# Kernel optimization log

Measured on AMD Instinct MI355X. Metric: run time of the kernel, lower is better.

Reference implementation:

```python
import jax, jax.numpy as jnp
import numpy as np

NB = 32          # num_basis
RMAX = 2.5       # max_radius
M0, M1 = 16, 8   # multiplicities of 0e and 1o irreps

# normalize2mom constant for silu (makes E[act(x)^2]=1 under N(0,1)), as in e3nn FullyConnectedNet
_p, _w = np.polynomial.hermite_e.hermegauss(128)
_s = _p / (1.0 + np.exp(-_p))
SILU_C = float(1.0 / np.sqrt((_w * _s * _s).sum() / np.sqrt(2.0 * np.pi)))

INV3 = 1.0 / np.sqrt(3.0)   # w3j(1,1,0)=w3j(0,1,1)=w3j(1,0,1) coefficient
INV6 = 1.0 / np.sqrt(6.0)   # w3j(1,1,1) = eps_ijk/sqrt(6)
PW0 = float(np.sqrt(1.0 / (M0 + M1)))        # path weight -> 0e (component/element norm)
PW1 = float(np.sqrt(3.0 / (M0 + M1 + M1)))   # path weight -> 1o
PW_SIM = float(np.sqrt(1.0 / (M0 * M0 + M1 * M1)))  # similarity TP path weight


def basis_net(rb, W1, W2):
    # e3nn FullyConnectedNet([NB,16,numel], silu): x@W/sqrt(fan_in), normalized act, linear out
    h = SILU_C * jax.nn.silu(rb @ (W1 / np.sqrt(NB)))
    return h @ (W2 / np.sqrt(16.0))


def fc_tp(x0, x1, sh0, sh1, w):
    # FullyConnectedTensorProduct (16x0e+8x1o) x (0e+1o) -> (16x0e+8x1o), per-edge weights
    # x0 [E,16], x1 [E,8,3], sh0 [E], sh1 [E,3], w [E,640]
    E = w.shape[0]
    w0 = w[:, 0:256].reshape(E, M0, M0)    # 0e x 0e -> 0e
    w1 = w[:, 256:384].reshape(E, M0, M1)  # 0e x 1o -> 1o
    w2 = w[:, 384:448].reshape(E, M1, M1)  # 1o x 0e -> 1o
    w3 = w[:, 448:576].reshape(E, M1, M0)  # 1o x 1o -> 0e
    w4 = w[:, 576:640].reshape(E, M1, M1)  # 1o x 1o -> 1o
    dot = jnp.einsum('eui,ei->eu', x1, sh1)
    out0 = PW0 * (jnp.einsum('euw,eu->ew', w0, x0 * sh0[:, None])
                  + INV3 * jnp.einsum('euw,eu->ew', w3, dot))
    crx = jnp.cross(x1, sh1[:, None, :])
    out1 = PW1 * (INV3 * jnp.einsum('euw,eu,ei->ewi', w1, x0, sh1)
                  + INV3 * sh0[:, None, None] * jnp.einsum('euw,eui->ewi', w2, x1)
                  + INV6 * jnp.einsum('euw,eui->ewi', w4, crx))
    return out0, out1


def forward(x, pos, edge_src, edge_dst, w_key1, w_key2, w_val1, w_val2, w_q0, w_q1, w_sim0, w_sim1):
    N = x.shape[0]
    x0 = x[:, :M0]                       # [N,16] scalars
    x1 = x[:, M0:].reshape(N, M1, 3)     # [N,8,3] vectors
    vec = pos[edge_src] - pos[edge_dst]  # [E,3]
    r = jnp.sqrt((vec * vec).sum(-1) + 1e-12)
    # bessel soft_one_hot_linspace with cutoff, scaled by sqrt(num_basis)
    n = jnp.arange(1, NB + 1, dtype=x.dtype) * jnp.pi
    rb = jnp.sqrt(2.0 / RMAX) * jnp.sin(n * (r[:, None] / RMAX)) / r[:, None]
    rb = jnp.where(r[:, None] < RMAX, rb, 0.0) * np.sqrt(1.0 * NB)
    # spherical harmonics lmax=1, normalize=True, normalization='component'
    unit = vec / r[:, None]
    sh0 = jnp.ones_like(r)
    sh1 = np.sqrt(3.0) * unit
    # query projection (o3.Linear, per-irrep dense / sqrt(fan_in))
    q0 = x0 @ (w_q0 / np.sqrt(M0))
    q1 = jnp.einsum('nui,uv->nvi', x1, w_q1) / np.sqrt(M1)
    x0s, x1s = x0[edge_src], x1[edge_src]
    k0, k1 = fc_tp(x0s, x1s, sh0, sh1, basis_net(rb, w_key1, w_key2))
    v0, v1 = fc_tp(x0s, x1s, sh0, sh1, basis_net(rb, w_val1, w_val2))
    # similarity TP (q,k)->0e
    s = PW_SIM * (jnp.einsum('eu,uv,ev->e', q0[edge_dst], w_sim0, k0)
                  + INV3 * jnp.einsum('eui,uv,evi->e', q1[edge_dst], w_sim1, k1))
    # scatter softmax over incoming edges per dst node
    smax = jax.ops.segment_max(s, edge_dst, num_segments=N)
    ex = jnp.exp(s - smax[edge_dst])
    attn = ex / jax.ops.segment_sum(ex, edge_dst, num_segments=N)[edge_dst]
    coef = jnp.sqrt(jax.nn.relu(attn))
    vals = jnp.concatenate([v0, v1.reshape(-1, 3 * M1)], axis=-1)  # [E,40]
    return jax.ops.segment_sum(coef[:, None] * vals, edge_dst, num_segments=N)


def setup_inputs() -> dict:
    key = jax.random.key(0)
    ks = jax.random.split(key, 12)
    N, E = 16384, 262144
    return dict(
        x=jax.random.normal(ks[0], (N, 40), jnp.float32),
        pos=jax.random.uniform(ks[1], (N, 3), jnp.float32) * 2.0,  # box so r spans cutoff
        edge_src=jax.random.randint(ks[2], (E,), 0, N, jnp.int32),
        edge_dst=jax.random.randint(ks[3], (E,), 0, N, jnp.int32),
        w_key1=jax.random.normal(ks[4], (32, 16), jnp.float32),
        w_key2=jax.random.normal(ks[5], (16, 640), jnp.float32),
        w_val1=jax.random.normal(ks[6], (32, 16), jnp.float32),
        w_val2=jax.random.normal(ks[7], (16, 640), jnp.float32),
        w_q0=jax.random.normal(ks[8], (16, 16), jnp.float32),
        w_q1=jax.random.normal(ks[9], (8, 8), jnp.float32),
        w_sim0=jax.random.normal(ks[10], (16, 16), jnp.float32),
        w_sim1=jax.random.normal(ks[11], (8, 8), jnp.float32),
    )


def reference(x, pos, edge_src, edge_dst, w_key1, w_key2, w_val1, w_val2, w_q0, w_q1, w_sim0, w_sim1):
    return forward(x, pos, edge_src, edge_dst, w_key1, w_key2, w_val1, w_val2, w_q0, w_q1, w_sim0, w_sim1)
```

## Files before the change

kernel.cpp:

```cpp
#include <hip/hip_runtime.h>
#include <math.h>

#define TPB 256
#define TPBF 192
#define SRCS_PER_GRP 8
#define SRC_STRIDE_U16 1928

#define RMAX_F 2.5f
#define PI_F 3.14159265358979323846f
#define SQRT3_F 1.7320508075688772f
#define INV3_F 0.5773502691896258f
#define INV6_F 0.4082482904638631f
#define PW0_F 0.2041241452319315f
#define PW1_F 0.3061862178478972f
#define PWSIM_F 0.05590169943749474f
#define SILU_C_F 1.676866f
#define RB_F 0.8944271909999159f
#define INV_SQRT8_F 0.35355339059327373f

typedef unsigned short u16t;
typedef _Float16 f16x2 __attribute__((ext_vector_type(2)));

#if defined(__has_builtin)
#if __has_builtin(__builtin_amdgcn_fdot2)
#define HAVE_FDOT2 1
#else
#define HAVE_FDOT2 0
#endif
#else
#define HAVE_FDOT2 0
#endif


__device__ __forceinline__ f16x2 as_f16x2(int v) {
  union { int i; f16x2 h; } u; u.i = v; return u.h;
}
__device__ __forceinline__ unsigned f16x2_bits(f16x2 h) {
  union { f16x2 h; unsigned u; } c; c.h = h; return c.u;
}
__device__ __forceinline__ float f16b2f(u16t b) {
  union { u16t u; _Float16 h; } c; c.u = b; return (float)c.h;
}

__device__ __forceinline__ float dot2f16(f16x2 a, f16x2 b, float c) {
#if HAVE_FDOT2
  return __builtin_amdgcn_fdot2(a, b, c, false);
#else
  return fmaf((float)a.x, (float)b.x, fmaf((float)a.y, (float)b.y, c));
#endif
}

__device__ __forceinline__ float dotjh(const u16t* __restrict__ t,
                                       const f16x2* __restrict__ hp) {
  const int4* q = reinterpret_cast<const int4*>(t);
  int4 a = q[0], b = q[1];
  float s0 = 0.f, s1 = 0.f;
  s0 = dot2f16(as_f16x2(a.x), hp[0], s0);
  s1 = dot2f16(as_f16x2(a.y), hp[1], s1);
  s0 = dot2f16(as_f16x2(a.z), hp[2], s0);
  s1 = dot2f16(as_f16x2(a.w), hp[3], s1);
  s0 = dot2f16(as_f16x2(b.x), hp[4], s0);
  s1 = dot2f16(as_f16x2(b.y), hp[5], s1);
  s0 = dot2f16(as_f16x2(b.z), hp[6], s0);
  s1 = dot2f16(as_f16x2(b.w), hp[7], s1);
  return s0 + s1;
}

__device__ __forceinline__ void pack_h16(const float* __restrict__ h,
                                         f16x2* __restrict__ hp) {
#pragma unroll
  for (int i = 0; i < 8; ++i) {
    f16x2 v;
    v.x = (_Float16)h[2 * i + 0];
    v.y = (_Float16)h[2 * i + 1];
    hp[i] = v;
  }
}

__device__ __forceinline__ float dot16u(const float* __restrict__ w, const float* __restrict__ h) {
  float a0 = 0.f, a1 = 0.f, a2 = 0.f, a3 = 0.f;
#pragma unroll
  for (int j = 0; j < 16; j += 4) {
    a0 = fmaf(h[j + 0], w[j + 0], a0);
    a1 = fmaf(h[j + 1], w[j + 1], a1);
    a2 = fmaf(h[j + 2], w[j + 2], a2);
    a3 = fmaf(h[j + 3], w[j + 3], a3);
  }
  return (a0 + a1) + (a2 + a3);
}

__device__ __forceinline__ void compute_h2s(const float* __restrict__ pos,
                                            const float* __restrict__ W1k,
                                            const float* __restrict__ W1v,
                                            int src, int dst,
                                            float& shx, float& shy, float& shz,
                                            float hk[16], float hv[16]) {
  float vx = pos[3 * src + 0] - pos[3 * dst + 0];
  float vy = pos[3 * src + 1] - pos[3 * dst + 1];
  float vz = pos[3 * src + 2] - pos[3 * dst + 2];
  float r2 = fmaf(vx, vx, fmaf(vy, vy, vz * vz)) + 1e-12f;
  float r = sqrtf(r2);
  float inv_r = 1.0f / r;
  shx = SQRT3_F * vx * inv_r;
  shy = SQRT3_F * vy * inv_r;
  shz = SQRT3_F * vz * inv_r;
  float f = (r < RMAX_F) ? (RB_F * inv_r) : 0.0f;
  float t0 = (PI_F / RMAX_F) * r;
  float s1, c1;
  __sincosf(t0, &s1, &c1);
  float c2 = 2.0f * c1;
  float sm = 0.0f, sc = s1;
  float ak[16], av[16];
#pragma unroll
  for (int j = 0; j < 16; ++j) { ak[j] = 0.0f; av[j] = 0.0f; }
#pragma unroll 2
  for (int n = 0; n < 32; ++n) {
    float rb = f * sc;
    const float* wk = W1k + n * 16;
    const float* wv = W1v + n * 16;
#pragma unroll
    for (int j = 0; j < 16; ++j) ak[j] = fmaf(rb, wk[j], ak[j]);
#pragma unroll
    for (int j = 0; j < 16; ++j) av[j] = fmaf(rb, wv[j], av[j]);
    float nx = fmaf(c2, sc, -sm);
    sm = sc; sc = nx;
  }
#pragma unroll
  for (int j = 0; j < 16; ++j) {
    float v = ak[j];
    hk[j] = SILU_C_F * v * (1.0f / (1.0f + __expf(-v)));
    float w = av[j];
    hv[j] = SILU_C_F * w * (1.0f / (1.0f + __expf(-w)));
  }
}

__device__ __forceinline__ void gen_entry_h(const u16t* __restrict__ W2H,
                                            const unsigned* __restrict__ xh,
                                            int mm, unsigned outw[8]) {
  f16x2 acc[8];
#pragma unroll
  for (int i = 0; i < 8; ++i) { acc[i].x = (_Float16)0.f; acc[i].y = (_Float16)0.f; }
  if (mm < 16) {
    int w = mm;
#pragma unroll 1
    for (int u = 0; u < 16; ++u) {
      f16x2 xv = as_f16x2((int)xh[u]);
      const f16x2* wp = reinterpret_cast<const f16x2*>(W2H + (u * 16 + w) * 16);
#pragma unroll
      for (int i = 0; i < 8; ++i) acc[i] += xv * wp[i];
    }
  } else if (mm < 24) {
    int w = mm - 16;
#pragma unroll 1
    for (int u = 0; u < 16; ++u) {
      f16x2 xv = as_f16x2((int)xh[u]);
      const f16x2* wp = reinterpret_cast<const f16x2*>(W2H + (256 + u * 8 + w) * 16);
#pragma unroll
      for (int i = 0; i < 8; ++i) acc[i] += xv * wp[i];
    }
  } else if (mm < 48) {
    int tt = mm - 24, w = tt / 3, i3 = tt - w * 3;
#pragma unroll 1
    for (int u = 0; u < 8; ++u) {
      f16x2 xv = as_f16x2((int)xh[16 + u * 3 + i3]);
      const f16x2* wp = reinterpret_cast<const f16x2*>(W2H + (384 + u * 8 + w) * 16);
#pragma unroll
      for (int i = 0; i < 8; ++i) acc[i] += xv * wp[i];
    }
  } else if (mm < 96) {
    int tt = mm - 48, w = tt / 3, i3 = tt - w * 3;
#pragma unroll 1
    for (int u = 0; u < 8; ++u) {
      f16x2 xv = as_f16x2((int)xh[16 + u * 3 + i3]);
      const f16x2* wp = reinterpret_cast<const f16x2*>(W2H + (448 + u * 16 + w) * 16);
#pragma unroll
      for (int i = 0; i < 8; ++i) acc[i] += xv * wp[i];
    }
  } else {
    int tt = mm - 96, w = tt / 3, i3 = tt - w * 3;
#pragma unroll 1
    for (int u = 0; u < 8; ++u) {
      f16x2 xv = as_f16x2((int)xh[16 + u * 3 + i3]);
      const f16x2* wp = reinterpret_cast<const f16x2*>(W2H + (576 + u * 8 + w) * 16);
#pragma unroll
      for (int i = 0; i < 8; ++i) acc[i] += xv * wp[i];
    }
  }
#pragma unroll
  for (int i = 0; i < 8; ++i) outw[i] = f16x2_bits(acc[i]);
}

__device__ __forceinline__ void gen_tables(const u16t* __restrict__ W2H,
                                           const unsigned* __restrict__ xh,
                                           u16t* __restrict__ tl,
                                           int nsrc, int tid) {
  for (int idx = tid; idx < nsrc * 120; idx += TPBF) {
    int m, s;
    if (nsrc == SRCS_PER_GRP) {
      m = idx >> 3;
      s = idx & 7;
    } else {
      m = idx / nsrc;
      s = idx - m * nsrc;
    }
    unsigned r[8];
    gen_entry_h(W2H, xh + s * 40, m, r);
    int4* dp = reinterpret_cast<int4*>(&tl[s * SRC_STRIDE_U16 + m * 16]);
    dp[0] = make_int4((int)r[0], (int)r[1], (int)r[2], (int)r[3]);
    dp[1] = make_int4((int)r[4], (int)r[5], (int)r[6], (int)r[7]);
  }
}


__global__ void k_prep(const float* __restrict__ wk2, const float* __restrict__ wv2,
                       const float* __restrict__ wq0, const float* __restrict__ wq1,
                       const float* __restrict__ ws0, const float* __restrict__ ws1,
                       float* __restrict__ W2Tk, float* __restrict__ W2Tv,
                       u16t* __restrict__ W2Hk, u16t* __restrict__ W2Hv,
                       float* __restrict__ C0, float* __restrict__ C1) {
  int i = blockIdx.x * blockDim.x + threadIdx.x;
  if (i < 10240) {
    int o = i >> 4, j = i & 15;
    float v = wk2[j * 640 + o] * 0.25f;
    W2Tk[i] = v;
    union { _Float16 h; u16t u; } c; c.h = (_Float16)v;
    W2Hk[i] = c.u;
  } else if (i < 20480) {
    int k = i - 10240;
    int o = k >> 4, j = k & 15;
    float v = wv2[j * 640 + o] * 0.25f;
    W2Tv[k] = v;
    union { _Float16 h; u16t u; } c; c.h = (_Float16)v;
    W2Hv[k] = c.u;
  } else if (i < 20736) {
    int k = i - 20480;
    int t = k >> 4, v = k & 15;
    float a = 0.f;
#pragma unroll
    for (int u = 0; u < 16; ++u) a = fmaf(wq0[t * 16 + u] * 0.25f, ws0[u * 16 + v], a);
    C0[k] = a;
  } else if (i < 20800) {
    int k = i - 20736;
    int t = k >> 3, v = k & 7;
    float a = 0.f;
#pragma unroll
    for (int u = 0; u < 8; ++u) a = fmaf(wq1[t * 8 + u] * INV_SQRT8_F, ws1[u * 8 + v], a);
    C1[k] = a;
  }
}

__global__ void k_node(const float* __restrict__ x, const float* __restrict__ C0,
                       const float* __restrict__ C1, float* __restrict__ qs0g,
                       float* __restrict__ qs1g, int N) {
  int n = blockIdx.x * blockDim.x + threadIdx.x;
  if (n >= N) return;
  float xr[40];
  const float4* p = reinterpret_cast<const float4*>(x + (size_t)n * 40);
#pragma unroll
  for (int q = 0; q < 10; ++q) {
    float4 v = p[q];
    xr[q * 4 + 0] = v.x; xr[q * 4 + 1] = v.y; xr[q * 4 + 2] = v.z; xr[q * 4 + 3] = v.w;
  }
  float o0[16];
#pragma unroll
  for (int v = 0; v < 16; ++v) o0[v] = 0.f;
#pragma unroll
  for (int t = 0; t < 16; ++t) {
    float xt = xr[t];
    const float* c = C0 + t * 16;
#pragma unroll
    for (int v = 0; v < 16; ++v) o0[v] = fmaf(xt, c[v], o0[v]);
  }
  float4* q0p = reinterpret_cast<float4*>(qs0g + (size_t)n * 16);
#pragma unroll
  for (int q = 0; q < 4; ++q)
    q0p[q] = make_float4(o0[q * 4], o0[q * 4 + 1], o0[q * 4 + 2], o0[q * 4 + 3]);

  float o1[24];
#pragma unroll
  for (int v = 0; v < 24; ++v) o1[v] = 0.f;
#pragma unroll
  for (int u = 0; u < 8; ++u) {
    const float* c = C1 + u * 8;
    float xa = xr[16 + u * 3 + 0], xb = xr[16 + u * 3 + 1], xc = xr[16 + u * 3 + 2];
#pragma unroll
    for (int v = 0; v < 8; ++v) {
      float cv = c[v];
      o1[v * 3 + 0] = fmaf(xa, cv, o1[v * 3 + 0]);
      o1[v * 3 + 1] = fmaf(xb, cv, o1[v * 3 + 1]);
      o1[v * 3 + 2] = fmaf(xc, cv, o1[v * 3 + 2]);
    }
  }
  float4* q1p = reinterpret_cast<float4*>(qs1g + (size_t)n * 24);
#pragma unroll
  for (int q = 0; q < 6; ++q)
    q1p[q] = make_float4(o1[q * 4], o1[q * 4 + 1], o1[q * 4 + 2], o1[q * 4 + 3]);
}


__global__ void k_hist2(const int* __restrict__ esrc, const int* __restrict__ edst,
                        int* __restrict__ cnt_s, int* __restrict__ cnt_d, int E) {
  int e = blockIdx.x * blockDim.x + threadIdx.x;
  if (e < E) {
    atomicAdd(&cnt_s[esrc[e]], 1);
    atomicAdd(&cnt_d[edst[e]], 1);
  }
}

__global__ void k_hist1(const int* __restrict__ key, int* __restrict__ cnt, int E) {
  int e = blockIdx.x * blockDim.x + threadIdx.x;
  if (e < E) atomicAdd(&cnt[key[e]], 1);
}

__global__ __launch_bounds__(1024) void k_scan2(const int* __restrict__ cnt_s,
                                                int* __restrict__ off_s,
                                                int* __restrict__ cur_s,
                                                const int* __restrict__ cnt_d,
                                                int* __restrict__ off_d,
                                                int* __restrict__ cur_d, int N) {
  const int* __restrict__ cnt = blockIdx.x ? cnt_d : cnt_s;
  int* __restrict__ off = blockIdx.x ? off_d : off_s;
  int* __restrict__ cur = blockIdx.x ? cur_d : cur_s;
  __shared__ int ls[1024];
  int tid = threadIdx.x;
  int per = (N + 1023) >> 10;
  int base = tid * per;
  int sum = 0;
  for (int j = 0; j < per; ++j) {
    int idx = base + j;
    if (idx < N) sum += cnt[idx];
  }
  ls[tid] = sum;
  __syncthreads();
  for (int d = 1; d < 1024; d <<= 1) {
    int v = (tid >= d) ? ls[tid - d] : 0;
    __syncthreads();
    ls[tid] += v;
    __syncthreads();
  }
  int run = ls[tid] - sum;
  for (int j = 0; j < per; ++j) {
    int idx = base + j;
    if (idx < N) {
      off[idx] = run;
      cur[idx] = run;
      run += cnt[idx];
    }
  }
  if (tid == 1023) off[N] = run;
}

__global__ void k_place2(const int* __restrict__ esrc, const int* __restrict__ edst,
                         int* __restrict__ cur_s, int* __restrict__ cur_d,
                         int* __restrict__ perm, int* __restrict__ idx, int E) {
  int e = blockIdx.x * blockDim.x + threadIdx.x;
  if (e < E) {
    int p = atomicAdd(&cur_s[esrc[e]], 1);
    perm[p] = e;
    int q = atomicAdd(&cur_d[edst[e]], 1);
    idx[q] = p;
  }
}

__global__ void k_place(const int* __restrict__ key, int* __restrict__ cursor,
                        int* __restrict__ perm, int E) {
  int e = blockIdx.x * blockDim.x + threadIdx.x;
  if (e < E) {
    int p = atomicAdd(&cursor[key[e]], 1);
    perm[p] = e;
  }
}


__global__ __launch_bounds__(TPBF) void k_fused(
    const float* __restrict__ x, const float* __restrict__ pos,
    const int* __restrict__ esrc, const int* __restrict__ edst,
    const int* __restrict__ perm, const int* __restrict__ off_s,
    const float* __restrict__ W1k, const u16t* __restrict__ W2Hk,
    const float* __restrict__ W1v, const u16t* __restrict__ W2Hv,
    const float* __restrict__ qs0g, const float* __restrict__ qs1g,
    float* __restrict__ s_out, u16t* __restrict__ stg, int N) {
  __shared__ __align__(16) u16t tl[SRCS_PER_GRP * SRC_STRIDE_U16];
  __shared__ unsigned xh[SRCS_PER_GRP * 40];
  int tid = threadIdx.x;
  int base = blockIdx.x * SRCS_PER_GRP;
  int nsrc = min(SRCS_PER_GRP, N - base);
  int glo = off_s[base], ghi = off_s[base + nsrc];

  for (int idx = tid; idx < nsrc * 40; idx += TPBF) {
    int s = idx / 40, u = idx - s * 40;
    float v = x[(size_t)(base + s) * 40 + u];
    f16x2 hh; hh.x = (_Float16)v; hh.y = hh.x;
    xh[s * 40 + u] = f16x2_bits(hh);
  }
  __syncthreads();

  gen_tables(W2Hk, xh, tl, nsrc, tid);
  __syncthreads();

  for (int p0 = glo; p0 < ghi; p0 += TPBF) {
    int p = p0 + tid;
    bool act = p < ghi;

    float shx = 0.f, shy = 0.f, shz = 0.f;
    int sloc = 0;
    f16x2 hvp[8];
#pragma unroll
    for (int j = 0; j < 8; ++j) { hvp[j].x = (_Float16)0.f; hvp[j].y = (_Float16)0.f; }

    if (act) {
      int e = perm[p];
      int src = esrc[e];
      int dst = edst[e];
      sloc = src - base;
      float hk[16], hv[16];
      compute_h2s(pos, W1k, W1v, src, dst, shx, shy, shz, hk, hv);
      f16x2 hkp[8];
      pack_h16(hk, hkp);
      pack_h16(hv, hvp);

      const u16t* tk = &tl[sloc * SRC_STRIDE_U16];
      const float4* q0p = reinterpret_cast<const float4*>(qs0g + (size_t)dst * 16);
      float S0 = 0.f;
#pragma unroll 2
      for (int w4 = 0; w4 < 4; ++w4) {
        float4 qq = q0p[w4];
        float q[4] = {qq.x, qq.y, qq.z, qq.w};
#pragma unroll
        for (int k = 0; k < 4; ++k) {
          float t0 = dotjh(tk + (w4 * 4 + k) * 16, hkp);
          float t3x = dotjh(tk + (48 + w4 * 12 + k * 3 + 0) * 16, hkp);
          float t3y = dotjh(tk + (48 + w4 * 12 + k * 3 + 1) * 16, hkp);
          float t3z = dotjh(tk + (48 + w4 * 12 + k * 3 + 2) * 16, hkp);
          S0 = fmaf(q[k], fmaf(INV3_F, t3x * shx + t3y * shy + t3z * shz, t0), S0);
        }
      }
      const float4* q1p = reinterpret_cast<const float4*>(qs1g + (size_t)dst * 24);
      float S1 = 0.f;
#pragma unroll 2
      for (int w4 = 0; w4 < 2; ++w4) {
        float4 qa = q1p[w4 * 3 + 0];
        float4 qb = q1p[w4 * 3 + 1];
        float4 qc = q1p[w4 * 3 + 2];
        float q[12] = {qa.x, qa.y, qa.z, qa.w, qb.x, qb.y, qb.z, qb.w,
                       qc.x, qc.y, qc.z, qc.w};
#pragma unroll
        for (int k = 0; k < 4; ++k) {
          float qx = q[k * 3 + 0], qy = q[k * 3 + 1], qz = q[k * 3 + 2];
          float t1 = dotjh(tk + (16 + w4 * 4 + k) * 16, hkp);
          float t2x = dotjh(tk + (24 + w4 * 12 + k * 3 + 0) * 16, hkp);
          float t2y = dotjh(tk + (24 + w4 * 12 + k * 3 + 1) * 16, hkp);
          float t2z = dotjh(tk + (24 + w4 * 12 + k * 3 + 2) * 16, hkp);
          float c0 = dotjh(tk + (96 + w4 * 12 + k * 3 + 0) * 16, hkp);
          float c1 = dotjh(tk + (96 + w4 * 12 + k * 3 + 1) * 16, hkp);
          float c2 = dotjh(tk + (96 + w4 * 12 + k * 3 + 2) * 16, hkp);
          float crx = c1 * shz - c2 * shy;
          float cry = c2 * shx - c0 * shz;
          float crz = c0 * shy - c1 * shx;
          float qdots = qx * shx + qy * shy + qz * shz;
          S1 += INV3_F * (t1 * qdots + t2x * qx + t2y * qy + t2z * qz) +
                INV6_F * (crx * qx + cry * qy + crz * qz);
        }
      }
      s_out[p] = PWSIM_F * (PW0_F * S0 + PW1_F * INV3_F * S1);
    }
    __syncthreads();

    gen_tables(W2Hv, xh, tl, nsrc, tid);
    __syncthreads();

    if (act) {
      const u16t* tv = &tl[sloc * SRC_STRIDE_U16];
      u16t* sp = stg + (size_t)p * 40;
#pragma unroll 2
      for (int w4 = 0; w4 < 4; ++w4) {
        float f[4];
#pragma unroll
        for (int k = 0; k < 4; ++k) {
          float t0 = dotjh(tv + (w4 * 4 + k) * 16, hvp);
          float t3x = dotjh(tv + (48 + w4 * 12 + k * 3 + 0) * 16, hvp);
          float t3y = dotjh(tv + (48 + w4 * 12 + k * 3 + 1) * 16, hvp);
          float t3z = dotjh(tv + (48 + w4 * 12 + k * 3 + 2) * 16, hvp);
          f[k] = PW0_F * fmaf(INV3_F, t3x * shx + t3y * shy + t3z * shz, t0);
        }
        f16x2 pa; pa.x = (_Float16)f[0]; pa.y = (_Float16)f[1];
        f16x2 pb; pb.x = (_Float16)f[2]; pb.y = (_Float16)f[3];
        int2 pk;
        pk.x = (int)f16x2_bits(pa);
        pk.y = (int)f16x2_bits(pb);
        *reinterpret_cast<int2*>(sp + w4 * 4) = pk;
      }
#pragma unroll 2
      for (int w4 = 0; w4 < 2; ++w4) {
        float f[12];
#pragma unroll
        for (int k = 0; k < 4; ++k) {
          float t1 = dotjh(tv + (16 + w4 * 4 + k) * 16, hvp);
          float t2x = dotjh(tv + (24 + w4 * 12 + k * 3 + 0) * 16, hvp);
          float t2y = dotjh(tv + (24 + w4 * 12 + k * 3 + 1) * 16, hvp);
          float t2z = dotjh(tv + (24 + w4 * 12 + k * 3 + 2) * 16, hvp);
          float c0 = dotjh(tv + (96 + w4 * 12 + k * 3 + 0) * 16, hvp);
          float c1 = dotjh(tv + (96 + w4 * 12 + k * 3 + 1) * 16, hvp);
          float c2 = dotjh(tv + (96 + w4 * 12 + k * 3 + 2) * 16, hvp);
          float crx = c1 * shz - c2 * shy;
          float cry = c2 * shx - c0 * shz;
          float crz = c0 * shy - c1 * shx;
          f[k * 3 + 0] = PW1_F * (INV3_F * fmaf(t1, shx, t2x) + INV6_F * crx);
          f[k * 3 + 1] = PW1_F * (INV3_F * fmaf(t1, shy, t2y) + INV6_F * cry);
          f[k * 3 + 2] = PW1_F * (INV3_F * fmaf(t1, shz, t2z) + INV6_F * crz);
        }
#pragma unroll
        for (int g = 0; g < 3; ++g) {
          f16x2 pa; pa.x = (_Float16)f[g * 4 + 0]; pa.y = (_Float16)f[g * 4 + 1];
          f16x2 pb; pb.x = (_Float16)f[g * 4 + 2]; pb.y = (_Float16)f[g * 4 + 3];
          int2 pk;
          pk.x = (int)f16x2_bits(pa);
          pk.y = (int)f16x2_bits(pb);
          *reinterpret_cast<int2*>(sp + 16 + w4 * 12 + g * 4) = pk;
        }
      }
    }

    if (p0 + TPBF < ghi) {
      __syncthreads();
      gen_tables(W2Hk, xh, tl, nsrc, tid);
      __syncthreads();
    }
  }
}


__global__ void k_smg(const float* __restrict__ s, const u16t* __restrict__ stg,
                      const int* __restrict__ off, const int* __restrict__ idx,
                      float* __restrict__ out, int N) {
  int gid = blockIdx.x * blockDim.x + threadIdx.x;
  int wid = gid >> 6;
  int lane = threadIdx.x & 63;
  if (wid >= N) return;
  int lo = off[wid], hi = off[wid + 1];
  float m = -1e30f;
  for (int q = lo + lane; q < hi; q += 64) m = fmaxf(m, s[idx[q]]);
#pragma unroll
  for (int d = 32; d; d >>= 1) m = fmaxf(m, __shfl_xor(m, d));
  float sum = 0.f;
  for (int q = lo + lane; q < hi; q += 64) sum += __expf(s[idx[q]] - m);
#pragma unroll
  for (int d = 32; d; d >>= 1) sum += __shfl_xor(sum, d);
  float inv = 1.0f / sum;
  float acc = 0.f;
  for (int q0 = lo; q0 < hi; q0 += 64) {
    int q = q0 + lane;
    int pv = 0;
    float cv = 0.f;
    if (q < hi) {
      pv = idx[q];
      cv = sqrtf(__expf(s[pv] - m) * inv);
    }
    int nj = min(64, hi - q0);
    for (int j = 0; j < nj; ++j) {
      float cj = __shfl(cv, j);
      int pj = __shfl(pv, j);
      if (lane < 40)
        acc = fmaf(cj, f16b2f(stg[(size_t)pj * 40 + lane]), acc);
    }
  }
  if (lane < 40) out[(size_t)wid * 40 + lane] = acc;
}


__global__ __launch_bounds__(TPB) void k_edge_fused(
    const float* __restrict__ x, const float* __restrict__ pos,
    const int* __restrict__ esrc, const int* __restrict__ edst,
    const int* __restrict__ perm,
    const float* __restrict__ W1k, const float* __restrict__ W2Tk,
    const float* __restrict__ W1v, const float* __restrict__ W2Tv,
    const float* __restrict__ qs0g, const float* __restrict__ qs1g,
    float* __restrict__ s_out, float* __restrict__ staging, int E) {
  __shared__ float xs[TPB * 41];
  int p = blockIdx.x * TPB + threadIdx.x;
  if (p >= E) return;
  int e = perm[p];
  int src = esrc[e], dst = edst[e];

  float* myx = &xs[threadIdx.x * 41];
  const float4* xrow = reinterpret_cast<const float4*>(x + (size_t)src * 40);
#pragma unroll
  for (int q = 0; q < 10; ++q) {
    float4 v = xrow[q];
    myx[q * 4 + 0] = v.x; myx[q * 4 + 1] = v.y; myx[q * 4 + 2] = v.z; myx[q * 4 + 3] = v.w;
  }

  float sh1[3], hk[16], hv[16];
  compute_h2s(pos, W1k, W1v, src, dst, sh1[0], sh1[1], sh1[2], hk, hv);

  {
    float qs0[16];
    {
      const float4* qp = reinterpret_cast<const float4*>(qs0g + (size_t)dst * 16);
#pragma unroll
      for (int q = 0; q < 4; ++q) {
        float4 v = qp[q];
        qs0[q * 4 + 0] = v.x; qs0[q * 4 + 1] = v.y; qs0[q * 4 + 2] = v.z; qs0[q * 4 + 3] = v.w;
      }
    }
    float qs1[24];
    {
      const float4* qp = reinterpret_cast<const float4*>(qs1g + (size_t)dst * 24);
#pragma unroll
      for (int q = 0; q < 6; ++q) {
        float4 v = qp[q];
        qs1[q * 4 + 0] = v.x; qs1[q * 4 + 1] = v.y; qs1[q * 4 + 2] = v.z; qs1[q * 4 + 3] = v.w;
      }
    }
    float qsh[8];
#pragma unroll
    for (int w = 0; w < 8; ++w)
      qsh[w] = qs1[w * 3] * sh1[0] + qs1[w * 3 + 1] * sh1[1] + qs1[w * 3 + 2] * sh1[2];

    float S0a = 0.f, S0b = 0.f, S1a = 0.f, S1b = 0.f, S1c = 0.f;
#pragma unroll 1
    for (int u = 0; u < 16; ++u) {
      const float* base = W2Tk + (u * 16) * 16;
      float accu = 0.f;
#pragma unroll
      for (int w = 0; w < 16; ++w) accu = fmaf(dot16u(base + w * 16, hk), qs0[w], accu);
      S0a = fmaf(accu, myx[u], S0a);
    }
#pragma unroll 1
    for (int u = 0; u < 16; ++u) {
      const float* base = W2Tk + (256 + u * 8) * 16;
      float accu = 0.f;
#pragma unroll
      for (int w = 0; w < 8; ++w) accu = fmaf(dot16u(base + w * 16, hk), qsh[w], accu);
      S1a = fmaf(accu, myx[u], S1a);
    }
#pragma unroll 1
    for (int u = 0; u < 8; ++u) {
      const float* base = W2Tk + (384 + u * 8) * 16;
      float x1a = myx[16 + u * 3 + 0], x1b = myx[16 + u * 3 + 1], x1c = myx[16 + u * 3 + 2];
      float accu = 0.f;
#pragma unroll
      for (int w = 0; w < 8; ++w) {
        float t = qs1[w * 3] * x1a + qs1[w * 3 + 1] * x1b + qs1[w * 3 + 2] * x1c;
        accu = fmaf(dot16u(base + w * 16, hk), t, accu);
      }
      S1b += accu;
    }
#pragma unroll 1
    for (int u = 0; u < 8; ++u) {
      const float* base = W2Tk + (448 + u * 16) * 16;
      float x1a = myx[16 + u * 3 + 0], x1b = myx[16 + u * 3 + 1], x1c = myx[16 + u * 3 + 2];
      float du = x1a * sh1[0] + x1b * sh1[1] + x1c * sh1[2];
      float accu = 0.f;
#pragma unroll
      for (int w = 0; w < 16; ++w) accu = fmaf(dot16u(base + w * 16, hk), qs0[w], accu);
      S0b = fmaf(accu, du, S0b);
    }
#pragma unroll 1
    for (int u = 0; u < 8; ++u) {
      const float* base = W2Tk + (576 + u * 8) * 16;
      float x1a = myx[16 + u * 3 + 0], x1b = myx[16 + u * 3 + 1], x1c = myx[16 + u * 3 + 2];
      float cx = x1b * sh1[2] - x1c * sh1[1];
      float cy = x1c * sh1[0] - x1a * sh1[2];
      float cz = x1a * sh1[1] - x1b * sh1[0];
      float accu = 0.f;
#pragma unroll
      for (int w = 0; w < 8; ++w) {
        float t = qs1[w * 3] * cx + qs1[w * 3 + 1] * cy + qs1[w * 3 + 2] * cz;
        accu = fmaf(dot16u(base + w * 16, hk), t, accu);
      }
      S1c += accu;
    }
    s_out[p] = PWSIM_F * (PW0_F * (S0a + INV3_F * S0b) +
                          (INV3_F * PW1_F) * (INV3_F * S1a + INV3_F * S1b + INV6_F * S1c));
  }

  float v0[16];
#pragma unroll
  for (int w = 0; w < 16; ++w) v0[w] = 0.f;
  float v1[24];
#pragma unroll
  for (int w = 0; w < 24; ++w) v1[w] = 0.f;

#pragma unroll 1
  for (int u = 0; u < 16; ++u) {
    const float* base = W2Tv + (u * 16) * 16;
    float xu = myx[u];
#pragma unroll
    for (int w = 0; w < 16; ++w) v0[w] = fmaf(dot16u(base + w * 16, hv), xu, v0[w]);
  }
  {
    float aw[8];
#pragma unroll
    for (int w = 0; w < 8; ++w) aw[w] = 0.f;
#pragma unroll 1
    for (int u = 0; u < 16; ++u) {
      const float* base = W2Tv + (256 + u * 8) * 16;
      float xu = myx[u];
#pragma unroll
      for (int w = 0; w < 8; ++w) aw[w] = fmaf(dot16u(base + w * 16, hv), xu, aw[w]);
    }
#pragma unroll
    for (int w = 0; w < 8; ++w) {
      float t = INV3_F * aw[w];
      v1[w * 3 + 0] = fmaf(t, sh1[0], v1[w * 3 + 0]);
      v1[w * 3 + 1] = fmaf(t, sh1[1], v1[w * 3 + 1]);
      v1[w * 3 + 2] = fmaf(t, sh1[2], v1[w * 3 + 2]);
    }
  }
#pragma unroll 1
  for (int u = 0; u < 8; ++u) {
    const float* base = W2Tv + (384 + u * 8) * 16;
    float a0 = INV3_F * myx[16 + u * 3 + 0];
    float a1 = INV3_F * myx[16 + u * 3 + 1];
    float a2 = INV3_F * myx[16 + u * 3 + 2];
#pragma unroll
    for (int w = 0; w < 8; ++w) {
      float wk = dot16u(base + w * 16, hv);
      v1[w * 3 + 0] = fmaf(wk, a0, v1[w * 3 + 0]);
      v1[w * 3 + 1] = fmaf(wk, a1, v1[w * 3 + 1]);
      v1[w * 3 + 2] = fmaf(wk, a2, v1[w * 3 + 2]);
    }
  }
#pragma unroll 1
  for (int u = 0; u < 8; ++u) {
    const float* base = W2Tv + (448 + u * 16) * 16;
    float x1a = myx[16 + u * 3 + 0], x1b = myx[16 + u * 3 + 1], x1c = myx[16 + u * 3 + 2];
    float du = INV3_F * (x1a * sh1[0] + x1b * sh1[1] + x1c * sh1[2]);
#pragma unroll
    for (int w = 0; w < 16; ++w) v0[w] = fmaf(dot16u(base + w * 16, hv), du, v0[w]);
  }
#pragma unroll 1
  for (int u = 0; u < 8; ++u) {
    const float* base = W2Tv + (576 + u * 8) * 16;
    float x1a = myx[16 + u * 3 + 0], x1b = myx[16 + u * 3 + 1], x1c = myx[16 + u * 3 + 2];
    float cx = INV6_F * (x1b * sh1[2] - x1c * sh1[1]);
    float cy = INV6_F * (x1c * sh1[0] - x1a * sh1[2]);
    float cz = INV6_F * (x1a * sh1[1] - x1b * sh1[0]);
#pragma unroll
    for (int w = 0; w < 8; ++w) {
      float wk = dot16u(base + w * 16, hv);
      v1[w * 3 + 0] = fmaf(wk, cx, v1[w * 3 + 0]);
      v1[w * 3 + 1] = fmaf(wk, cy, v1[w * 3 + 1]);
      v1[w * 3 + 2] = fmaf(wk, cz, v1[w * 3 + 2]);
    }
  }

  float outv[40];
#pragma unroll
  for (int w = 0; w < 16; ++w) outv[w] = PW0_F * v0[w];
#pragma unroll
  for (int w = 0; w < 24; ++w) outv[16 + w] = PW1_F * v1[w];
  float4* st = reinterpret_cast<float4*>(staging + (size_t)p * 40);
#pragma unroll
  for (int q = 0; q < 10; ++q)
    st[q] = make_float4(outv[q * 4], outv[q * 4 + 1], outv[q * 4 + 2], outv[q * 4 + 3]);
}

__global__ void k_softmax(const float* __restrict__ s, const int* __restrict__ off,
                          float* __restrict__ coef, int N) {
  int gid = blockIdx.x * blockDim.x + threadIdx.x;
  int wid = gid >> 6;
  int lane = threadIdx.x & 63;
  if (wid >= N) return;
  int lo = off[wid], hi = off[wid + 1];
  float m = -1e30f;
  for (int p = lo + lane; p < hi; p += 64) m = fmaxf(m, s[p]);
#pragma unroll
  for (int d = 32; d; d >>= 1) m = fmaxf(m, __shfl_xor(m, d));
  float sum = 0.f;
  for (int p = lo + lane; p < hi; p += 64) sum += __expf(s[p] - m);
#pragma unroll
  for (int d = 32; d; d >>= 1) sum += __shfl_xor(sum, d);
  float inv = 1.0f / sum;
  for (int p = lo + lane; p < hi; p += 64)
    coef[p] = sqrtf(__expf(s[p] - m) * inv);
}

__global__ void k_gather(const float* __restrict__ staging, const float* __restrict__ coef,
                         const int* __restrict__ off, float* __restrict__ out, int N) {
  int gid = blockIdx.x * blockDim.x + threadIdx.x;
  int wid = gid >> 6;
  int lane = threadIdx.x & 63;
  if (wid >= N) return;
  int lo = off[wid], hi = off[wid + 1];
  if (lane < 40) {
    float acc = 0.f;
    for (int p = lo; p < hi; ++p)
      acc = fmaf(coef[p], staging[(size_t)p * 40 + lane], acc);
    out[(size_t)wid * 40 + lane] = acc;
  }
}


extern "C" void kernel_launch(void* const* d_in, const int* in_sizes, int n_in,
                              void* d_out, int out_size, void* d_ws, size_t ws_size,
                              hipStream_t stream) {
  const float* x   = (const float*)d_in[0];
  const float* pos = (const float*)d_in[1];
  const int* esrc  = (const int*)d_in[2];
  const int* edst  = (const int*)d_in[3];
  const float* wk1 = (const float*)d_in[4];
  const float* wk2 = (const float*)d_in[5];
  const float* wv1 = (const float*)d_in[6];
  const float* wv2 = (const float*)d_in[7];
  const float* wq0 = (const float*)d_in[8];
  const float* wq1 = (const float*)d_in[9];
  const float* ws0 = (const float*)d_in[10];
  const float* ws1 = (const float*)d_in[11];

  int E = in_sizes[2];
  int N = in_sizes[0] / 40;

  float* ws = (float*)d_ws;
  float* W2Tk = ws;
  float* W2Tv = ws + 10240;
  float* C0   = ws + 20480;
  float* C1   = ws + 20736;
  u16t* W2Hk  = (u16t*)(ws + 20800);
  u16t* W2Hv  = W2Hk + 10240;
  float* qs0g = ws + 20800 + 10240;
  float* qs1g = qs0g + (size_t)N * 16;
  float* base2 = qs1g + (size_t)N * 24;

  float* s_ws = base2;
  int* cnt_s  = (int*)(s_ws + (size_t)E);
  int* cnt_d  = cnt_s + N;
  int* off_s  = cnt_d + N;
  int* cur_s  = off_s + N + 1;
  int* off_d  = cur_s + N;
  int* cur_d  = off_d + N + 1;
  int* perm   = cur_d + N;
  int* idxd   = perm + (size_t)E;
  u16t* stgb  = (u16t*)(idxd + (size_t)E);
  size_t need_fast = (size_t)((char*)(stgb + (size_t)E * 40) - (char*)d_ws);

  k_prep<<<(20800 + 255) / 256, 256, 0, stream>>>(wk2, wv2, wq0, wq1, ws0, ws1,
                                                  W2Tk, W2Tv, W2Hk, W2Hv, C0, C1);
  k_node<<<(N + 255) / 256, 256, 0, stream>>>(x, C0, C1, qs0g, qs1g, N);

  if (ws_size >= need_fast) {
    hipMemsetAsync(cnt_s, 0, sizeof(int) * (size_t)(2 * N), stream);
    k_hist2<<<(E + 255) / 256, 256, 0, stream>>>(esrc, edst, cnt_s, cnt_d, E);
    k_scan2<<<2, 1024, 0, stream>>>(cnt_s, off_s, cur_s, cnt_d, off_d, cur_d, N);
    k_place2<<<(E + 255) / 256, 256, 0, stream>>>(esrc, edst, cur_s, cur_d,
                                                  perm, idxd, E);
    int ng = (N + SRCS_PER_GRP - 1) / SRCS_PER_GRP;
    k_fused<<<ng, TPBF, 0, stream>>>(x, pos, esrc, edst, perm, off_s,
                                     wk1, W2Hk, wv1, W2Hv, qs0g, qs1g,
                                     s_ws, stgb, N);
    k_smg<<<((N * 64) + 255) / 256, 256, 0, stream>>>(s_ws, stgb, off_d, idxd,
                                                      (float*)d_out, N);
  } else {
    float* coefF = s_ws + (size_t)E;
    int* cnt    = (int*)(coefF + (size_t)E);
    int* off    = cnt + N;
    int* cursor = off + N + 1;
    int* permF  = cursor + N;
    float* staging = (float*)(permF + (size_t)E);

    hipMemsetAsync(cnt, 0, sizeof(int) * (size_t)N, stream);
    k_hist1<<<(E + 255) / 256, 256, 0, stream>>>(edst, cnt, E);
    k_scan2<<<1, 1024, 0, stream>>>(cnt, off, cursor, cnt, off, cursor, N);
    k_place<<<(E + 255) / 256, 256, 0, stream>>>(edst, cursor, permF, E);
    k_edge_fused<<<(E + TPB - 1) / TPB, TPB, 0, stream>>>(
        x, pos, esrc, edst, permF, wk1, W2Tk, wv1, W2Tv, qs0g, qs1g,
        s_ws, staging, E);
    k_softmax<<<((N * 64) + 255) / 256, 256, 0, stream>>>(s_ws, off, coefF, N);
    k_gather<<<((N * 64) + 255) / 256, 256, 0, stream>>>(staging, coefF, off,
                                                         (float*)d_out, N);
  }
}
```

Baseline: 248.9 us.

## Merge prep/hist and scan/node launches; store sorted src/dst instead of perm

Folds the weight-prep kernel into the histogram kernel and the node projection kernel into the scan kernel as extra blocks, which cuts two launches and lets independent work share each launch. The place kernel now writes the source-sorted src and dst indices directly, so the fused edge kernel reads them contiguously instead of going through a permutation gather. The cost is one extra E-sized int array of workspace and writes. Node blocks now use 1024 threads, which may lower occupancy for the register-heavy node body.

```diff
diff --git a/kernel.cpp b/kernel.cpp
--- a/kernel.cpp
+++ b/kernel.cpp
@@ -212,13 +212,13 @@
 }
 
 
-__global__ void k_prep(const float* __restrict__ wk2, const float* __restrict__ wv2,
-                       const float* __restrict__ wq0, const float* __restrict__ wq1,
-                       const float* __restrict__ ws0, const float* __restrict__ ws1,
-                       float* __restrict__ W2Tk, float* __restrict__ W2Tv,
-                       u16t* __restrict__ W2Hk, u16t* __restrict__ W2Hv,
-                       float* __restrict__ C0, float* __restrict__ C1) {
-  int i = blockIdx.x * blockDim.x + threadIdx.x;
+__device__ __forceinline__ void prep_body(int i,
+    const float* __restrict__ wk2, const float* __restrict__ wv2,
+    const float* __restrict__ wq0, const float* __restrict__ wq1,
+    const float* __restrict__ ws0, const float* __restrict__ ws1,
+    float* __restrict__ W2Tk, float* __restrict__ W2Tv,
+    u16t* __restrict__ W2Hk, u16t* __restrict__ W2Hv,
+    float* __restrict__ C0, float* __restrict__ C1) {
   if (i < 10240) {
     int o = i >> 4, j = i & 15;
     float v = wk2[j * 640 + o] * 0.25f;
@@ -249,11 +249,42 @@
   }
 }
 
-__global__ void k_node(const float* __restrict__ x, const float* __restrict__ C0,
-                       const float* __restrict__ C1, float* __restrict__ qs0g,
-                       float* __restrict__ qs1g, int N) {
-  int n = blockIdx.x * blockDim.x + threadIdx.x;
-  if (n >= N) return;
+__global__ void k_prep(const float* __restrict__ wk2, const float* __restrict__ wv2,
+                       const float* __restrict__ wq0, const float* __restrict__ wq1,
+                       const float* __restrict__ ws0, const float* __restrict__ ws1,
+                       float* __restrict__ W2Tk, float* __restrict__ W2Tv,
+                       u16t* __restrict__ W2Hk, u16t* __restrict__ W2Hv,
+                       float* __restrict__ C0, float* __restrict__ C1) {
+  int i = blockIdx.x * blockDim.x + threadIdx.x;
+  prep_body(i, wk2, wv2, wq0, wq1, ws0, ws1, W2Tk, W2Tv, W2Hk, W2Hv, C0, C1);
+}
+
+__global__ void k_hist_prep(const int* __restrict__ esrc, const int* __restrict__ edst,
+                            int* __restrict__ cnt_s, int* __restrict__ cnt_d, int E,
+                            int histBlocks,
+                            const float* __restrict__ wk2, const float* __restrict__ wv2,
+                            const float* __restrict__ wq0, const float* __restrict__ wq1,
+                            const float* __restrict__ ws0, const float* __restrict__ ws1,
+                            float* __restrict__ W2Tk, float* __restrict__ W2Tv,
+                            u16t* __restrict__ W2Hk, u16t* __restrict__ W2Hv,
+                            float* __restrict__ C0, float* __restrict__ C1) {
+  if ((int)blockIdx.x < histBlocks) {
+    int e = blockIdx.x * blockDim.x + threadIdx.x;
+    if (e < E) {
+      atomicAdd(&cnt_s[esrc[e]], 1);
+      atomicAdd(&cnt_d[edst[e]], 1);
+    }
+  } else {
+    int i = (blockIdx.x - histBlocks) * blockDim.x + threadIdx.x;
+    prep_body(i, wk2, wv2, wq0, wq1, ws0, ws1, W2Tk, W2Tv, W2Hk, W2Hv, C0, C1);
+  }
+}
+
+__device__ __forceinline__ void node_body(int n, const float* __restrict__ x,
+                                          const float* __restrict__ C0,
+                                          const float* __restrict__ C1,
+                                          float* __restrict__ qs0g,
+                                          float* __restrict__ qs1g) {
   float xr[40];
   const float4* p = reinterpret_cast<const float4*>(x + (size_t)n * 40);
 #pragma unroll
@@ -297,19 +328,61 @@
     q1p[q] = make_float4(o1[q * 4], o1[q * 4 + 1], o1[q * 4 + 2], o1[q * 4 + 3]);
 }
 
-
-__global__ void k_hist2(const int* __restrict__ esrc, const int* __restrict__ edst,
-                        int* __restrict__ cnt_s, int* __restrict__ cnt_d, int E) {
-  int e = blockIdx.x * blockDim.x + threadIdx.x;
-  if (e < E) {
-    atomicAdd(&cnt_s[esrc[e]], 1);
-    atomicAdd(&cnt_d[edst[e]], 1);
-  }
-}
+__global__ void k_node(const float* __restrict__ x, const float* __restrict__ C0,
+                       const float* __restrict__ C1, float* __restrict__ qs0g,
+                       float* __restrict__ qs1g, int N) {
+  int n = blockIdx.x * blockDim.x + threadIdx.x;
+  if (n < N) node_body(n, x, C0, C1, qs0g, qs1g);
+}
+
 
 __global__ void k_hist1(const int* __restrict__ key, int* __restrict__ cnt, int E) {
   int e = blockIdx.x * blockDim.x + threadIdx.x;
   if (e < E) atomicAdd(&cnt[key[e]], 1);
+}
+
+__global__ __launch_bounds__(1024) void k_scan_node(
+    const int* __restrict__ cnt_s, int* __restrict__ off_s, int* __restrict__ cur_s,
+    const int* __restrict__ cnt_d, int* __restrict__ off_d, int* __restrict__ cur_d,
+    int N,
+    const float* __restrict__ x, const float* __restrict__ C0,
+    const float* __restrict__ C1, float* __restrict__ qs0g,
+    float* __restrict__ qs1g) {
+  __shared__ int ls[1024];
+  if (blockIdx.x < 2) {
+    const int* __restrict__ cnt = blockIdx.x ? cnt_d : cnt_s;
+    int* __restrict__ off = blockIdx.x ? off_d : off_s;
+    int* __restrict__ cur = blockIdx.x ? cur_d : cur_s;
+    int tid = threadIdx.x;
+    int per = (N + 1023) >> 10;
+    int base = tid * per;
+    int sum = 0;
+    for (int j = 0; j < per; ++j) {
+      int idx = base + j;
+      if (idx < N) sum += cnt[idx];
+    }
+    ls[tid] = sum;
+    __syncthreads();
+    for (int d = 1; d < 1024; d <<= 1) {
+      int v = (tid >= d) ? ls[tid - d] : 0;
+      __syncthreads();
+      ls[tid] += v;
+      __syncthreads();
+    }
+    int run = ls[tid] - sum;
+    for (int j = 0; j < per; ++j) {
+      int idx = base + j;
+      if (idx < N) {
+        off[idx] = run;
+        cur[idx] = run;
+        run += cnt[idx];
+      }
+    }
+    if (tid == 1023) off[N] = run;
+  } else {
+    int n = (blockIdx.x - 2) * 1024 + threadIdx.x;
+    if (n < N) node_body(n, x, C0, C1, qs0g, qs1g);
+  }
 }
 
 __global__ __launch_bounds__(1024) void k_scan2(const int* __restrict__ cnt_s,
@@ -350,14 +423,17 @@
   if (tid == 1023) off[N] = run;
 }
 
-__global__ void k_place2(const int* __restrict__ esrc, const int* __restrict__ edst,
+__global__ void k_place3(const int* __restrict__ esrc, const int* __restrict__ edst,
                          int* __restrict__ cur_s, int* __restrict__ cur_d,
-                         int* __restrict__ perm, int* __restrict__ idx, int E) {
+                         int* __restrict__ es2, int* __restrict__ ed2,
+                         int* __restrict__ idx, int E) {
   int e = blockIdx.x * blockDim.x + threadIdx.x;
   if (e < E) {
-    int p = atomicAdd(&cur_s[esrc[e]], 1);
-    perm[p] = e;
-    int q = atomicAdd(&cur_d[edst[e]], 1);
+    int s = esrc[e], d = edst[e];
+    int p = atomicAdd(&cur_s[s], 1);
+    es2[p] = s;
+    ed2[p] = d;
+    int q = atomicAdd(&cur_d[d], 1);
     idx[q] = p;
   }
 }
@@ -374,8 +450,8 @@
 
 __global__ __launch_bounds__(TPBF) void k_fused(
     const float* __restrict__ x, const float* __restrict__ pos,
-    const int* __restrict__ esrc, const int* __restrict__ edst,
-    const int* __restrict__ perm, const int* __restrict__ off_s,
+    const int* __restrict__ es2, const int* __restrict__ ed2,
+    const int* __restrict__ off_s,
     const float* __restrict__ W1k, const u16t* __restrict__ W2Hk,
     const float* __restrict__ W1v, const u16t* __restrict__ W2Hv,
     const float* __restrict__ qs0g, const float* __restrict__ qs1g,
@@ -409,9 +485,8 @@
     for (int j = 0; j < 8; ++j) { hvp[j].x = (_Float16)0.f; hvp[j].y = (_Float16)0.f; }
 
     if (act) {
-      int e = perm[p];
-      int src = esrc[e];
-      int dst = edst[e];
+      int src = es2[p];
+      int dst = ed2[p];
       sloc = src - base;
       float hk[16], hv[16];
       compute_h2s(pos, W1k, W1v, src, dst, shx, shy, shz, hk, hv);
@@ -830,23 +905,26 @@
   int* cur_s  = off_s + N + 1;
   int* off_d  = cur_s + N;
   int* cur_d  = off_d + N + 1;
-  int* perm   = cur_d + N;
-  int* idxd   = perm + (size_t)E;
+  int* es2    = cur_d + N;
+  int* ed2    = es2 + (size_t)E;
+  int* idxd   = ed2 + (size_t)E;
   u16t* stgb  = (u16t*)(idxd + (size_t)E);
   size_t need_fast = (size_t)((char*)(stgb + (size_t)E * 40) - (char*)d_ws);
 
-  k_prep<<<(20800 + 255) / 256, 256, 0, stream>>>(wk2, wv2, wq0, wq1, ws0, ws1,
-                                                  W2Tk, W2Tv, W2Hk, W2Hv, C0, C1);
-  k_node<<<(N + 255) / 256, 256, 0, stream>>>(x, C0, C1, qs0g, qs1g, N);
-
   if (ws_size >= need_fast) {
     hipMemsetAsync(cnt_s, 0, sizeof(int) * (size_t)(2 * N), stream);
-    k_hist2<<<(E + 255) / 256, 256, 0, stream>>>(esrc, edst, cnt_s, cnt_d, E);
-    k_scan2<<<2, 1024, 0, stream>>>(cnt_s, off_s, cur_s, cnt_d, off_d, cur_d, N);
-    k_place2<<<(E + 255) / 256, 256, 0, stream>>>(esrc, edst, cur_s, cur_d,
-                                                  perm, idxd, E);
+    int histBlocks = (E + 255) / 256;
+    int prepBlocks = (20800 + 255) / 256;
+    k_hist_prep<<<histBlocks + prepBlocks, 256, 0, stream>>>(
+        esrc, edst, cnt_s, cnt_d, E, histBlocks,
+        wk2, wv2, wq0, wq1, ws0, ws1, W2Tk, W2Tv, W2Hk, W2Hv, C0, C1);
+    int nodeBlocks = (N + 1023) / 1024;
+    k_scan_node<<<2 + nodeBlocks, 1024, 0, stream>>>(
+        cnt_s, off_s, cur_s, cnt_d, off_d, cur_d, N, x, C0, C1, qs0g, qs1g);
+    k_place3<<<(E + 255) / 256, 256, 0, stream>>>(esrc, edst, cur_s, cur_d,
+                                                  es2, ed2, idxd, E);
     int ng = (N + SRCS_PER_GRP - 1) / SRCS_PER_GRP;
-    k_fused<<<ng, TPBF, 0, stream>>>(x, pos, esrc, edst, perm, off_s,
+    k_fused<<<ng, TPBF, 0, stream>>>(x, pos, es2, ed2, off_s,
                                      wk1, W2Hk, wv1, W2Hv, qs0g, qs1g,
                                      s_ws, stgb, N);
     k_smg<<<((N * 64) + 255) / 256, 256, 0, stream>>>(s_ws, stgb, off_d, idxd,
@@ -859,6 +937,9 @@
     int* permF  = cursor + N;
     float* staging = (float*)(permF + (size_t)E);
 
+    k_prep<<<(20800 + 255) / 256, 256, 0, stream>>>(wk2, wv2, wq0, wq1, ws0, ws1,
+                                                    W2Tk, W2Tv, W2Hk, W2Hv, C0, C1);
+    k_node<<<(N + 255) / 256, 256, 0, stream>>>(x, C0, C1, qs0g, qs1g, N);
     hipMemsetAsync(cnt, 0, sizeof(int) * (size_t)N, stream);
     k_hist1<<<(E + 255) / 256, 256, 0, stream>>>(edst, cnt, E);
     k_scan2<<<1, 1024, 0, stream>>>(cnt, off, cursor, cnt, off, cursor, N);
```

Result: faster. 240.2 us (median of 2 runs) (-3.5%).
